# Optimization experiments

Hardware: AMD Instinct MI355X
Metric: run time of the kernel (lower is better)

Reference implementation:

```python
import jax, jax.numpy as jnp
import numpy as np

B, S, D = 64, 2048, 64  # (batch*heads, seq_len, head_dim)

def setup_inputs() -> dict:
    key = jax.random.key(0)
    kq, kk, kv = jax.random.split(key, 3)
    q = jax.random.normal(kq, (B, S, D), dtype=jnp.float32)
    k = jax.random.normal(kk, (B, S, D), dtype=jnp.float32)
    v = jax.random.normal(kv, (B, S, D), dtype=jnp.float32)
    return {"q": q, "k": k, "v": v}

def reference(q, k, v):
    # scores: [B, S, S] = q @ k^T (no scaling, matching the source module)
    scores = jnp.einsum('bqd,bkd->bqk', q, k)
    attn = jax.nn.softmax(scores, axis=-1)
    # dropout p=0.0 -> identity
    out = jnp.einsum('bqk,bkd->bqd', attn, v)
    return out
```

## Files before the change

### kernel.cpp

```cpp
#include <hip/hip_runtime.h>

typedef __attribute__((ext_vector_type(8))) __bf16 bf16x8;
typedef __attribute__((ext_vector_type(8))) _Float16 f16x8;
typedef __attribute__((ext_vector_type(4))) float f32x4;
typedef __attribute__((ext_vector_type(8))) unsigned short u16x8;

#define SDIM 2048
#define DDIM 64
#define NBATCH 64
#define LOG2E 1.44269504088896340736f

#if __has_builtin(__builtin_amdgcn_exp2f)
#define EXP2F __builtin_amdgcn_exp2f
#else
#define EXP2F exp2f
#endif

__device__ inline unsigned short f2bf(float f) {
  unsigned u = __builtin_bit_cast(unsigned, f);
  u += 0x7fffu + ((u >> 16) & 1u);
  return (unsigned short)(u >> 16);
}
__device__ inline unsigned short f2h(float f) {
  return __builtin_bit_cast(unsigned short, (_Float16)f);
}

__device__ inline void gload_lds16(const void* g, void* l) {
  __builtin_amdgcn_global_load_lds(
      (const __attribute__((address_space(1))) unsigned int*)g,
      (__attribute__((address_space(3))) unsigned int*)l, 16, 0, 0);
}

__device__ inline int rperm(int p) { return p ^ ((p >> 3) & 7); }

__global__ __launch_bounds__(256) void prep_kernel(
    const float* __restrict__ k, const float* __restrict__ v,
    unsigned short* __restrict__ khf, unsigned short* __restrict__ vtb) {
  __shared__ float tile[64][65];
  const int b = blockIdx.x >> 5;
  const int s0 = (blockIdx.x & 31) * 64;
  const size_t base = ((size_t)b * SDIM + s0) * DDIM;

  {
    const float* src = k + base + threadIdx.x * 16;
    f32x4 a = *(const f32x4*)src;
    f32x4 b4 = *(const f32x4*)(src + 4);
    f32x4 c4 = *(const f32x4*)(src + 8);
    f32x4 d4 = *(const f32x4*)(src + 12);
    u16x8 o0, o1;
#pragma unroll
    for (int j = 0; j < 4; ++j) {
      o0[j] = f2h(a[j] * LOG2E);
      o0[4 + j] = f2h(b4[j] * LOG2E);
      o1[j] = f2h(c4[j] * LOG2E);
      o1[4 + j] = f2h(d4[j] * LOG2E);
    }
    unsigned short* dst = khf + base + threadIdx.x * 16;
    *(u16x8*)dst = o0;
    *(u16x8*)(dst + 8) = o1;
  }

  {
    int row = threadIdx.x >> 2;
    int c16 = (threadIdx.x & 3) * 16;
    const float* src = v + base + (size_t)row * DDIM + c16;
#pragma unroll
    for (int c = 0; c < 4; ++c) {
      f32x4 f = *(const f32x4*)(src + 4 * c);
      tile[row][c16 + 4 * c + 0] = f[0];
      tile[row][c16 + 4 * c + 1] = f[1];
      tile[row][c16 + 4 * c + 2] = f[2];
      tile[row][c16 + 4 * c + 3] = f[3];
    }
    __syncthreads();
    int d = threadIdx.x >> 2;
    int sc = (threadIdx.x & 3) * 16;
    u16x8 a, c;
#pragma unroll
    for (int j = 0; j < 8; ++j) a[j] = f2bf(tile[sc + j][d]);
#pragma unroll
    for (int j = 0; j < 8; ++j) c[j] = f2bf(tile[sc + 8 + j][d]);
    unsigned short* dst = vtb + ((size_t)b * DDIM + d) * SDIM + s0 + sc;
    *(u16x8*)dst = a;
    *(u16x8*)(dst + 8) = c;
  }
}

__global__ __launch_bounds__(256, 2) void attn_kernel(
    const float* __restrict__ q, const unsigned short* __restrict__ khf,
    const unsigned short* __restrict__ vt, float* __restrict__ out) {
  __shared__ __align__(16) unsigned short kv[2 * 16 * 512];
  __shared__ __align__(16) unsigned short pf[4 * 8 * 512];

  const int bid = blockIdx.x;
  const int b = (bid & 7) * 8 + (bid >> 6);
  const int qt = (bid >> 3) & 7;
  const int tid = threadIdx.x;
  const int w = tid >> 6;
  const int L = tid & 63;
  const int l15 = L & 15;
  const int l4 = L >> 4;

  const size_t boff = (size_t)b * (SDIM * DDIM);
  const int qg = qt * 256 + w * 64;

  f16x8 qa[4][2];
#pragma unroll
  for (int t = 0; t < 4; ++t)
#pragma unroll
    for (int c = 0; c < 2; ++c) {
      const float* src = q + boff + (size_t)(qg + t * 16 + l15) * DDIM + c * 32 + l4 * 8;
      f32x4 f0 = *(const f32x4*)(src);
      f32x4 f1 = *(const f32x4*)(src + 4);
      f16x8 h;
#pragma unroll
      for (int j = 0; j < 4; ++j) {
        h[j] = (_Float16)f0[j];
        h[4 + j] = (_Float16)f1[j];
      }
      qa[t][c] = h;
    }

  u16x8 uo;
#pragma unroll
  for (int j = 0; j < 8; ++j) uo[j] = 0x3F80;
  const bf16x8 ones = __builtin_bit_cast(bf16x8, uo);

  int pw[2][4];
#pragma unroll
  for (int n1 = 0; n1 < 2; ++n1)
#pragma unroll
    for (int r = 0; r < 4; ++r) {
      int lane2 = l4 * 4 + r + (n1 * 2 + (l15 >> 3)) * 16;
      pw[n1][r] = rperm(lane2) * 8 + (L & 7);
    }
  const int prd = rperm(L) * 8;
  unsigned short* pwave = pf + w * 4096;

  const unsigned short* gsrc[4];
  int gadv;
  if (w < 2) {
#pragma unroll
    for (int ff = 0; ff < 4; ++ff) {
      int f = w * 4 + ff;
      gsrc[ff] = khf + boff + (size_t)((f >> 1) * 16 + l15) * DDIM + (f & 1) * 32 + l4 * 8;
    }
    gadv = 64 * DDIM;
  } else {
#pragma unroll
    for (int ff = 0; ff < 4; ++ff) {
      int fg = (w - 2) * 4 + ff;
      gsrc[ff] = vt + boff + (size_t)((fg >> 1) * 16 + l15) * SDIM + (fg & 1) * 32 + l4 * 8;
    }
    gadv = 64;
  }
  const int fdbase = w * 4;

  f32x4 o[4][4], lacc[4];
#pragma unroll
  for (int t = 0; t < 4; ++t) {
#pragma unroll
    for (int n = 0; n < 4; ++n) o[t][n] = (f32x4){0.f, 0.f, 0.f, 0.f};
    lacc[t] = (f32x4){0.f, 0.f, 0.f, 0.f};
  }

#pragma unroll
  for (int ff = 0; ff < 4; ++ff) gload_lds16(gsrc[ff], &kv[(fdbase + ff) * 512]);
#pragma unroll
  for (int ff = 0; ff < 4; ++ff) gsrc[ff] += gadv;

  for (int it = 0; it < SDIM / 64; ++it) {
    const int cur = it & 1;
    __syncthreads();
    if (it + 1 < SDIM / 64) {
#pragma unroll
      for (int ff = 0; ff < 4; ++ff)
        gload_lds16(gsrc[ff], &kv[(1 - cur) * 8192 + (fdbase + ff) * 512]);
#pragma unroll
      for (int ff = 0; ff < 4; ++ff) gsrc[ff] += gadv;
    }
    const unsigned short* kvc = &kv[cur * 8192];

#pragma unroll
    for (int n = 0; n < 4; ++n) {
      f16x8 k0 = *(const f16x8*)&kvc[(n * 2 + 0) * 512 + L * 8];
      f16x8 k1 = *(const f16x8*)&kvc[(n * 2 + 1) * 512 + L * 8];
#pragma unroll
      for (int t = 0; t < 4; ++t) {
        f32x4 acc = (f32x4){0.f, 0.f, 0.f, 0.f};
        acc = __builtin_amdgcn_mfma_f32_16x16x32_f16(qa[t][0], k0, acc, 0, 0, 0);
        acc = __builtin_amdgcn_mfma_f32_16x16x32_f16(qa[t][1], k1, acc, 0, 0, 0);
        int fp = (t * 2 + (n >> 1)) * 512;
#pragma unroll
        for (int r = 0; r < 4; ++r) {
          float p = EXP2F(acc[r]);
          unsigned u = __builtin_bit_cast(unsigned, p);
          pwave[fp + pw[n & 1][r]] = (unsigned short)((u + 0x8000u) >> 16);
        }
      }
    }

#pragma unroll
    for (int t = 0; t < 4; ++t) {
      bf16x8 p0 = *(const bf16x8*)&pwave[(t * 2 + 0) * 512 + prd];
      bf16x8 p1 = *(const bf16x8*)&pwave[(t * 2 + 1) * 512 + prd];
      lacc[t] = __builtin_amdgcn_mfma_f32_16x16x32_bf16(p0, ones, lacc[t], 0, 0, 0);
      lacc[t] = __builtin_amdgcn_mfma_f32_16x16x32_bf16(p1, ones, lacc[t], 0, 0, 0);
#pragma unroll
      for (int n = 0; n < 4; ++n) {
        bf16x8 v0 = *(const bf16x8*)&kvc[(8 + n * 2 + 0) * 512 + L * 8];
        bf16x8 v1 = *(const bf16x8*)&kvc[(8 + n * 2 + 1) * 512 + L * 8];
        o[t][n] = __builtin_amdgcn_mfma_f32_16x16x32_bf16(p0, v0, o[t][n], 0, 0, 0);
        o[t][n] = __builtin_amdgcn_mfma_f32_16x16x32_bf16(p1, v1, o[t][n], 0, 0, 0);
      }
    }
  }

#pragma unroll
  for (int t = 0; t < 4; ++t) {
    float rc[4];
#pragma unroll
    for (int r = 0; r < 4; ++r) rc[r] = 1.f / lacc[t][r];
#pragma unroll
    for (int n = 0; n < 4; ++n)
#pragma unroll
      for (int r = 0; r < 4; ++r)
        out[boff + (size_t)(qg + t * 16 + l4 * 4 + r) * DDIM + n * 16 + l15] =
            o[t][n][r] * rc[r];
  }
}

extern "C" void kernel_launch(void* const* d_in, const int* in_sizes, int n_in,
                              void* d_out, int out_size, void* d_ws, size_t ws_size,
                              hipStream_t stream) {
  const float* q = (const float*)d_in[0];
  const float* k = (const float*)d_in[1];
  const float* v = (const float*)d_in[2];
  float* out = (float*)d_out;
  unsigned short* khf = (unsigned short*)d_ws;
  unsigned short* vt = khf + (size_t)NBATCH * SDIM * DDIM;

  prep_kernel<<<NBATCH * (SDIM / 64), 256, 0, stream>>>(k, v, khf, vt);
  attn_kernel<<<NBATCH * (SDIM / 256), 256, 0, stream>>>(q, khf, vt, out);
}
```

Baseline: 225.4 us.

## Transpose QK MFMA to pack P writes and replace ones-MFMA rowsum with register sums

Swaps the MFMA operand order so each lane holds four consecutive keys for one query row. This lets the probabilities be packed into a single 8-byte LDS store instead of four scattered 2-byte stores, and drops the swizzle tables. The row sum is now accumulated in fp32 registers and reduced with shuffles at the end, which removes the extra ones-vector MFMAs per tile. V fragments are also hoisted out of the t loop and loaded once per iteration, at the cost of more registers and possible LDS bank conflicts from the unswizzled layout.

```diff
diff --git a/kernel.cpp b/kernel.cpp
--- a/kernel.cpp
+++ b/kernel.cpp
@@ -4,6 +4,7 @@
 typedef __attribute__((ext_vector_type(8))) _Float16 f16x8;
 typedef __attribute__((ext_vector_type(4))) float f32x4;
 typedef __attribute__((ext_vector_type(8))) unsigned short u16x8;
+typedef __attribute__((ext_vector_type(2))) unsigned int u32x2;
 
 #define SDIM 2048
 #define DDIM 64
@@ -30,8 +31,6 @@
       (const __attribute__((address_space(1))) unsigned int*)g,
       (__attribute__((address_space(3))) unsigned int*)l, 16, 0, 0);
 }
-
-__device__ inline int rperm(int p) { return p ^ ((p >> 3) & 7); }
 
 __global__ __launch_bounds__(256) void prep_kernel(
     const float* __restrict__ k, const float* __restrict__ v,
@@ -104,7 +103,7 @@
   const size_t boff = (size_t)b * (SDIM * DDIM);
   const int qg = qt * 256 + w * 64;
 
-  f16x8 qa[4][2];
+  f16x8 qb[4][2];
 #pragma unroll
   for (int t = 0; t < 4; ++t)
 #pragma unroll
@@ -118,23 +117,10 @@
         h[j] = (_Float16)f0[j];
         h[4 + j] = (_Float16)f1[j];
       }
-      qa[t][c] = h;
-    }
-
-  u16x8 uo;
-#pragma unroll
-  for (int j = 0; j < 8; ++j) uo[j] = 0x3F80;
-  const bf16x8 ones = __builtin_bit_cast(bf16x8, uo);
-
-  int pw[2][4];
-#pragma unroll
-  for (int n1 = 0; n1 < 2; ++n1)
-#pragma unroll
-    for (int r = 0; r < 4; ++r) {
-      int lane2 = l4 * 4 + r + (n1 * 2 + (l15 >> 3)) * 16;
-      pw[n1][r] = rperm(lane2) * 8 + (L & 7);
-    }
-  const int prd = rperm(L) * 8;
+      qb[t][c] = h;
+    }
+
+  const int pwoff = (l15 + 16 * (l4 >> 1)) * 8 + 4 * (l4 & 1);
   unsigned short* pwave = pf + w * 4096;
 
   const unsigned short* gsrc[4];
@@ -156,12 +142,13 @@
   }
   const int fdbase = w * 4;
 
-  f32x4 o[4][4], lacc[4];
+  f32x4 o[4][4];
+  float lsum[4];
 #pragma unroll
   for (int t = 0; t < 4; ++t) {
 #pragma unroll
     for (int n = 0; n < 4; ++n) o[t][n] = (f32x4){0.f, 0.f, 0.f, 0.f};
-    lacc[t] = (f32x4){0.f, 0.f, 0.f, 0.f};
+    lsum[t] = 0.f;
   }
 
 #pragma unroll
@@ -182,45 +169,54 @@
     const unsigned short* kvc = &kv[cur * 8192];
 
 #pragma unroll
-    for (int n = 0; n < 4; ++n) {
-      f16x8 k0 = *(const f16x8*)&kvc[(n * 2 + 0) * 512 + L * 8];
-      f16x8 k1 = *(const f16x8*)&kvc[(n * 2 + 1) * 512 + L * 8];
+    for (int nt = 0; nt < 4; ++nt) {
+      f16x8 k0 = *(const f16x8*)&kvc[(nt * 2 + 0) * 512 + L * 8];
+      f16x8 k1 = *(const f16x8*)&kvc[(nt * 2 + 1) * 512 + L * 8];
+      const int pbase = (nt >> 1) * 512 + pwoff + (nt & 1) * 256;
 #pragma unroll
       for (int t = 0; t < 4; ++t) {
         f32x4 acc = (f32x4){0.f, 0.f, 0.f, 0.f};
-        acc = __builtin_amdgcn_mfma_f32_16x16x32_f16(qa[t][0], k0, acc, 0, 0, 0);
-        acc = __builtin_amdgcn_mfma_f32_16x16x32_f16(qa[t][1], k1, acc, 0, 0, 0);
-        int fp = (t * 2 + (n >> 1)) * 512;
-#pragma unroll
-        for (int r = 0; r < 4; ++r) {
-          float p = EXP2F(acc[r]);
-          unsigned u = __builtin_bit_cast(unsigned, p);
-          pwave[fp + pw[n & 1][r]] = (unsigned short)((u + 0x8000u) >> 16);
-        }
+        acc = __builtin_amdgcn_mfma_f32_16x16x32_f16(k0, qb[t][0], acc, 0, 0, 0);
+        acc = __builtin_amdgcn_mfma_f32_16x16x32_f16(k1, qb[t][1], acc, 0, 0, 0);
+        float p0 = EXP2F(acc[0]), p1 = EXP2F(acc[1]);
+        float p2 = EXP2F(acc[2]), p3 = EXP2F(acc[3]);
+        lsum[t] += (p0 + p1) + (p2 + p3);
+        unsigned a0 = __builtin_bit_cast(unsigned, p0) + 0x8000u;
+        unsigned a1 = __builtin_bit_cast(unsigned, p1) + 0x8000u;
+        unsigned a2 = __builtin_bit_cast(unsigned, p2) + 0x8000u;
+        unsigned a3 = __builtin_bit_cast(unsigned, p3) + 0x8000u;
+        u32x2 wv;
+        wv[0] = __builtin_amdgcn_perm(a1, a0, 0x07060302u);
+        wv[1] = __builtin_amdgcn_perm(a3, a2, 0x07060302u);
+        *(u32x2*)&pwave[t * 1024 + pbase] = wv;
       }
     }
 
+    bf16x8 vv[8];
+#pragma unroll
+    for (int i = 0; i < 8; ++i) vv[i] = *(const bf16x8*)&kvc[(8 + i) * 512 + L * 8];
 #pragma unroll
     for (int t = 0; t < 4; ++t) {
-      bf16x8 p0 = *(const bf16x8*)&pwave[(t * 2 + 0) * 512 + prd];
-      bf16x8 p1 = *(const bf16x8*)&pwave[(t * 2 + 1) * 512 + prd];
-      lacc[t] = __builtin_amdgcn_mfma_f32_16x16x32_bf16(p0, ones, lacc[t], 0, 0, 0);
-      lacc[t] = __builtin_amdgcn_mfma_f32_16x16x32_bf16(p1, ones, lacc[t], 0, 0, 0);
+      bf16x8 p0 = *(const bf16x8*)&pwave[(t * 2 + 0) * 512 + L * 8];
+      bf16x8 p1 = *(const bf16x8*)&pwave[(t * 2 + 1) * 512 + L * 8];
 #pragma unroll
       for (int n = 0; n < 4; ++n) {
-        bf16x8 v0 = *(const bf16x8*)&kvc[(8 + n * 2 + 0) * 512 + L * 8];
-        bf16x8 v1 = *(const bf16x8*)&kvc[(8 + n * 2 + 1) * 512 + L * 8];
-        o[t][n] = __builtin_amdgcn_mfma_f32_16x16x32_bf16(p0, v0, o[t][n], 0, 0, 0);
-        o[t][n] = __builtin_amdgcn_mfma_f32_16x16x32_bf16(p1, v1, o[t][n], 0, 0, 0);
+        o[t][n] = __builtin_amdgcn_mfma_f32_16x16x32_bf16(p0, vv[n * 2 + 0], o[t][n], 0, 0, 0);
+        o[t][n] = __builtin_amdgcn_mfma_f32_16x16x32_bf16(p1, vv[n * 2 + 1], o[t][n], 0, 0, 0);
       }
     }
   }
 
+#pragma unroll
+  for (int t = 0; t < 4; ++t) {
+    lsum[t] += __shfl_xor(lsum[t], 16);
+    lsum[t] += __shfl_xor(lsum[t], 32);
+  }
 #pragma unroll
   for (int t = 0; t < 4; ++t) {
     float rc[4];
 #pragma unroll
-    for (int r = 0; r < 4; ++r) rc[r] = 1.f / lacc[t][r];
+    for (int r = 0; r < 4; ++r) rc[r] = 1.f / __shfl(lsum[t], l4 * 4 + r);
 #pragma unroll
     for (int n = 0; n < 4; ++n)
 #pragma unroll
```

Result: faster. 215.5 us (-4.4%).
